# Optimization experiments

Measured on AMD Instinct MI355X. Metric: run time of the kernel, lower is better.

## Reference

```python
import jax, jax.numpy as jnp
import numpy as np

DIM = 1024
HEADS = 16
DIM_HEAD = 64
NUM_FREQS = 16
INNER = HEADS * DIM_HEAD


def rotate_half(x):
    # matches torch: cat((-x[..., 1::2], x[..., ::2]), dim=-1)
    x1 = x[..., ::2]
    x2 = x[..., 1::2]
    return jnp.concatenate((-x2, x1), axis=-1)


def rope_fourier_cache(seq_len, head_dim, num_freqs):
    freqs = 10000.0 ** (-jnp.arange(0, head_dim, 2, dtype=jnp.float32) / head_dim)  # [hd/2]
    pos = jnp.arange(seq_len, dtype=jnp.float32)[:, None]  # [n,1]
    angles = pos * freqs  # [n, hd/2]
    sin = jnp.sin(angles)
    cos = jnp.cos(angles)
    # interleave-duplicate each value per pair: [n, hd]
    sin = jnp.stack([sin, sin], axis=-1).reshape(seq_len, head_dim)
    cos = jnp.stack([cos, cos], axis=-1).reshape(seq_len, head_dim)
    ffreqs = jnp.arange(1, num_freqs + 1, dtype=jnp.float32)  # [F]
    p = jnp.arange(seq_len, dtype=jnp.float32)[:, None]  # [n,1]
    fourier = jnp.concatenate([jnp.sin(p * ffreqs), jnp.cos(p * ffreqs)], axis=-1)  # [n, 2F]
    return sin, cos, fourier


def setup_inputs() -> dict:
    key = jax.random.key(0)
    ks = jax.random.split(key, 6)
    b, n = 4, 2048
    x = jax.random.normal(ks[0], (b, n, DIM), dtype=jnp.float32)
    w_qkv = jax.random.normal(ks[1], (3 * INNER, DIM), dtype=jnp.float32) * (DIM ** -0.5)
    w_fproj = jax.random.normal(ks[2], (DIM_HEAD, 2 * NUM_FREQS), dtype=jnp.float32) * ((2 * NUM_FREQS) ** -0.5)
    b_fproj = jax.random.normal(ks[3], (DIM_HEAD,), dtype=jnp.float32) * 0.02
    w_out = jax.random.normal(ks[4], (DIM, INNER), dtype=jnp.float32) * (INNER ** -0.5)
    b_out = jax.random.normal(ks[5], (DIM,), dtype=jnp.float32) * 0.02
    return {"x": x, "w_qkv": w_qkv, "w_fproj": w_fproj, "b_fproj": b_fproj,
            "w_out": w_out, "b_out": b_out}


def reference(x, w_qkv, w_fproj, b_fproj, w_out, b_out):
    b, n, _ = x.shape
    scale = DIM_HEAD ** -0.5
    qkv = x @ w_qkv.T  # [b, n, 3*inner]
    q, k, v = jnp.split(qkv, 3, axis=-1)
    def to_heads(t):
        return t.reshape(b, n, HEADS, DIM_HEAD).transpose(0, 2, 1, 3)  # [b,h,n,d]
    q, k, v = to_heads(q), to_heads(k), to_heads(v)
    sin, cos, fourier = rope_fourier_cache(n, DIM_HEAD, NUM_FREQS)
    fenc = fourier @ w_fproj.T + b_fproj  # [n, d]
    fenc = fenc[None, None]  # [1,1,n,d]
    q = q * cos + rotate_half(q) * sin + fenc
    k = k * cos + rotate_half(k) * sin + fenc
    dots = jnp.einsum('bhid,bhjd->bhij', q, k) * scale
    attn = jax.nn.softmax(dots, axis=-1)
    out = jnp.einsum('bhij,bhjd->bhid', attn, v)
    out = out.transpose(0, 2, 1, 3).reshape(b, n, INNER)
    return out @ w_out.T + b_out
```

## Files before the change

### kernel.cpp

```cpp
#include <hip/hip_runtime.h>
#include <math.h>

#define NB 4
#define SEQ 2048
#define DIMM 1024
#define NH 16
#define DHD 64
#define NFQ 16

typedef __bf16 bf16x8 __attribute__((ext_vector_type(8)));
typedef __bf16 bf16x4 __attribute__((ext_vector_type(4)));
typedef float f32x4 __attribute__((ext_vector_type(4)));
typedef float f32x16 __attribute__((ext_vector_type(16)));
typedef unsigned int u32x4 __attribute__((ext_vector_type(4)));

#if __has_builtin(__builtin_amdgcn_exp2f)
#define EXP2F(x) __builtin_amdgcn_exp2f(x)
#else
#define EXP2F(x) exp2f(x)
#endif

__device__ inline unsigned short f2bf(float f) {
  unsigned int u = __builtin_bit_cast(unsigned int, f);
  u += 0x7fffu + ((u >> 16) & 1u);
  return (unsigned short)(u >> 16);
}

#define GLL16(gp, lp) __builtin_amdgcn_global_load_lds( \
    (__attribute__((address_space(1))) void*)(gp), \
    (__attribute__((address_space(3))) void*)(lp), 16, 0, 0)

__global__ __launch_bounds__(64) void rope_tab_kernel(const float* __restrict__ w_fproj,
                                                      const float* __restrict__ b_fproj,
                                                      float4* __restrict__ tab) {
  const int pos = blockIdx.x;
  const int d = threadIdx.x;
  __shared__ float four[2 * NFQ];
  if (d < NFQ) {
    double a = (double)pos * (double)(d + 1);
    four[d] = (float)sin(a);
    four[d + NFQ] = (float)cos(a);
  }
  __syncthreads();
  float fe = b_fproj[d];
  const float* wr = w_fproj + d * 2 * NFQ;
#pragma unroll
  for (int j = 0; j < 2 * NFQ; ++j) fe += four[j] * wr[j];
  const int i = d >> 1;
  const double freq = exp(((double)(-2 * i)) / 64.0 * log(10000.0));
  const float angle = (float)pos * (float)freq;
  const float c = (float)cos((double)angle);
  const float s = (float)sin((double)angle);
  tab[(pos << 6) + d] = make_float4(c, s, fe, 0.f);
}

__global__ __launch_bounds__(256) void f2bf_kernel(const float* __restrict__ src,
                                                   unsigned short* __restrict__ dst, int n4) {
  for (int i = blockIdx.x * 256 + threadIdx.x; i < n4; i += gridDim.x * 256) {
    const float4 v = ((const float4*)src)[i];
    ushort4 o;
    o.x = f2bf(v.x); o.y = f2bf(v.y); o.z = f2bf(v.z); o.w = f2bf(v.w);
    ((ushort4*)dst)[i] = o;
  }
}

template<int EPI>
__global__ __launch_bounds__(256) void gemm_bt(const unsigned short* __restrict__ A,
                                               const unsigned short* __restrict__ Bw,
                                               int K,
                                               float* __restrict__ outF,
                                               unsigned short* __restrict__ outQ,
                                               unsigned short* __restrict__ outK,
                                               unsigned short* __restrict__ outV,
                                               const float4* __restrict__ tab,
                                               const float* __restrict__ bias,
                                               float qscale) {
  __shared__ __align__(16) unsigned short As[3][128 * 32];
  __shared__ __align__(16) unsigned short Bs[3][128 * 32];
  const int t = threadIdx.x, l = t & 63, w = t >> 6;
  const int wr = w >> 1, wc = w & 1;
  const int orig = blockIdx.x + gridDim.x * blockIdx.y;
  const int xcd = orig & 7, idx = orig >> 3;
  const int sc = idx >> 5, r5 = idx & 31;
  const int bm = ((xcd << 3) + (r5 >> 2)) * 128;
  const int bn = ((sc << 2) + (r5 & 3)) * 128;
  const f32x4 z = {0.f, 0.f, 0.f, 0.f};
  f32x4 acc[4][4];
#pragma unroll
  for (int m = 0; m < 4; ++m)
#pragma unroll
    for (int n = 0; n < 4; ++n) acc[m][n] = z;

  auto stage = [&](int k0, int buf) {
#pragma unroll
    for (int j = 0; j < 2; ++j) {
      const int Bb = w * 2048 + j * 1024 + l * 16;
      const int row = Bb >> 6, bin = Bb & 63;
      const int sb = bin ^ ((row & 3) << 4);
      GLL16(A  + (size_t)(bm + row) * K + k0 + (sb >> 1), (char*)(&As[buf][0]) + w * 2048 + j * 1024);
      GLL16(Bw + (size_t)(bn + row) * K + k0 + (sb >> 1), (char*)(&Bs[buf][0]) + w * 2048 + j * 1024);
    }
  };

  const int NT = K >> 5;
  stage(0, 0);
  if (NT > 1) stage(32, 1);
  if (NT > 2) stage(64, 2);
  int cur = 0;
  for (int it = 0; it < NT; ++it) {
    const int rem = NT - 1 - it;
    if (rem >= 2)      asm volatile("s_waitcnt vmcnt(8)" ::: "memory");
    else if (rem == 1) asm volatile("s_waitcnt vmcnt(4)" ::: "memory");
    else               asm volatile("s_waitcnt vmcnt(0)" ::: "memory");
    __builtin_amdgcn_s_barrier();

    bf16x8 af[4], bfr[4];
#pragma unroll
    for (int m = 0; m < 4; ++m) {
      const int row = wr * 64 + m * 16 + (l & 15);
      const int bin = ((l >> 4) * 16) ^ ((row & 3) << 4);
      af[m] = *(const bf16x8*)((const char*)(&As[cur][0]) + row * 64 + bin);
    }
#pragma unroll
    for (int n = 0; n < 4; ++n) {
      const int row = wc * 64 + n * 16 + (l & 15);
      const int bin = ((l >> 4) * 16) ^ ((row & 3) << 4);
      bfr[n] = *(const bf16x8*)((const char*)(&Bs[cur][0]) + row * 64 + bin);
    }
#pragma unroll
    for (int m = 0; m < 4; ++m)
#pragma unroll
      for (int n = 0; n < 4; ++n)
        acc[m][n] = __builtin_amdgcn_mfma_f32_16x16x32_bf16(af[m], bfr[n], acc[m][n], 0, 0, 0);

    asm volatile("s_waitcnt lgkmcnt(0)" ::: "memory");
    __builtin_amdgcn_s_barrier();
    if (it + 3 < NT) stage((it + 3) * 32, cur);
    cur = (cur == 2) ? 0 : cur + 1;
  }

  const int c = l & 15;
  if (EPI == 0) {
    const int which = bn >> 10;
    const int h = ((bn & 1023) >> 6) + wc;
    if (which == 2) {
#pragma unroll
      for (int m = 0; m < 4; ++m)
#pragma unroll
        for (int n = 0; n < 4; ++n) {
          const int d = n * 16 + c;
#pragma unroll
          for (int r = 0; r < 4; ++r) {
            const int mrow = bm + wr * 64 + m * 16 + (l >> 4) * 4 + r;
            const int b = mrow >> 11, pos = mrow & (SEQ - 1);
            outV[((size_t)(b * NH + h) * DHD + d) * SEQ + pos] = f2bf(acc[m][n][r]);
          }
        }
    } else {
      unsigned short* dst = (which == 0) ? outQ : outK;
      const float sc2 = (which == 0) ? qscale : 1.f;
      const int laneE = (l & 48) | ((2 * c) & 15);
      const int laneO = (l & 48) | ((2 * c + 1) & 15);
      const bool hi = (c >= 8);
#pragma unroll
      for (int m = 0; m < 4; ++m)
#pragma unroll
        for (int r = 0; r < 4; ++r) {
          const int mrow = bm + wr * 64 + m * 16 + (l >> 4) * 4 + r;
          const int b = mrow >> 11, pos = mrow & (SEQ - 1);
          const float V0 = acc[m][0][r], V1 = acc[m][1][r];
          const float V2 = acc[m][2][r], V3 = acc[m][3][r];
          const float e0 = __shfl(V0, laneE), e1 = __shfl(V1, laneE);
          const float e2 = __shfl(V2, laneE), e3 = __shfl(V3, laneE);
          const float o0 = __shfl(V0, laneO), o1 = __shfl(V1, laneO);
          const float o2 = __shfl(V2, laneO), o3 = __shfl(V3, laneO);
          const float rot0 = -(hi ? o1 : o0);
          const float rot1 = -(hi ? o3 : o2);
          const float rot2 =  (hi ? e1 : e0);
          const float rot3 =  (hi ? e3 : e2);
          const float4 t0 = tab[(pos << 6) + c];
          const float4 t1 = tab[(pos << 6) + 16 + c];
          const float4 t2 = tab[(pos << 6) + 32 + c];
          const float4 t3 = tab[(pos << 6) + 48 + c];
          unsigned short* drow = dst + ((size_t)(b * NH + h) * SEQ + pos) * DHD + c;
          drow[0]  = f2bf((V0 * t0.x + rot0 * t0.y + t0.z) * sc2);
          drow[16] = f2bf((V1 * t1.x + rot1 * t1.y + t1.z) * sc2);
          drow[32] = f2bf((V2 * t2.x + rot2 * t2.y + t2.z) * sc2);
          drow[48] = f2bf((V3 * t3.x + rot3 * t3.y + t3.z) * sc2);
        }
    }
  } else {
#pragma unroll
    for (int m = 0; m < 4; ++m)
#pragma unroll
      for (int n = 0; n < 4; ++n) {
        const int ncol = bn + wc * 64 + n * 16 + c;
        const float bb = bias[ncol];
#pragma unroll
        for (int r = 0; r < 4; ++r) {
          const int mrow = bm + wr * 64 + m * 16 + (l >> 4) * 4 + r;
          outF[(size_t)mrow * DIMM + ncol] = acc[m][n][r] + bb;
        }
      }
  }
}

__global__ __launch_bounds__(256, 2) void attn_kernel(const unsigned short* __restrict__ qbf,
                                                      const unsigned short* __restrict__ kbf,
                                                      const unsigned short* __restrict__ vt,
                                                      unsigned short* __restrict__ ao) {
  __shared__ __align__(16) unsigned short Ks[2][64 * 64], Vts[2][64 * 64];
  __shared__ float ltab[4][64];
  const int t = threadIdx.x, l = t & 63, w = t >> 6;
  const int G = l >> 5, c32 = l & 31;
  int flat = blockIdx.x + (blockIdx.y << 3);
  flat = (flat & 7) * 64 + (flat >> 3);
  const int q0 = (flat & 7) * 256;
  const int bh = flat >> 3;
  const int b = bh >> 4, h = bh & 15;
  const size_t hbase = (size_t)bh * SEQ * DHD;
  const int woff = w * 64;

  auto stageKV = [&](int kt, int buf) {
#pragma unroll
    for (int j = 0; j < 2; ++j) {
      const int base = (w * 2 + j) * 1024;
      const int row = (base + l * 16) >> 7;
      const int sb = ((l & 7) * 16) ^ ((row & 7) << 4);
      GLL16(kbf + hbase + (size_t)(kt + row) * DHD + (sb >> 1),
            (char*)(&Ks[buf][0]) + base);
      GLL16(vt  + hbase + (size_t)row * SEQ + kt + (sb >> 1),
            (char*)(&Vts[buf][0]) + base);
    }
  };

  bf16x8 qf[2][4];
#pragma unroll
  for (int qg = 0; qg < 2; ++qg)
#pragma unroll
    for (int j = 0; j < 4; ++j)
      qf[qg][j] = *(const bf16x8*)(qbf + hbase +
          (size_t)(q0 + woff + qg * 32 + c32) * DHD + 16 * j + 8 * G);

  stageKV(0, 0);
  stageKV(64, 1);

  f32x16 of[2][2];
  float psum[2] = {0.f, 0.f};
#pragma unroll
  for (int qg = 0; qg < 2; ++qg)
#pragma unroll
    for (int dg = 0; dg < 2; ++dg)
#pragma unroll
      for (int r = 0; r < 16; ++r) of[qg][dg][r] = 0.f;

  for (int kt = 0; kt < SEQ; kt += 64) {
    const int cur = (kt >> 6) & 1;
    if (kt + 64 < SEQ) asm volatile("s_waitcnt vmcnt(4)" ::: "memory");
    else               asm volatile("s_waitcnt vmcnt(0)" ::: "memory");
    __builtin_amdgcn_s_barrier();

    const char* Kc = (const char*)(&Ks[cur][0]);
    const char* Vc = (const char*)(&Vts[cur][0]);

#pragma unroll
    for (int ksub = 0; ksub < 2; ++ksub) {
      f32x16 sf0, sf1;
#pragma unroll
      for (int r = 0; r < 16; ++r) { sf0[r] = 0.f; sf1[r] = 0.f; }
      const int krow = ksub * 32 + c32;
      const int kswz = (krow & 7) << 4;
      __builtin_amdgcn_s_setprio(1);
#pragma unroll
      for (int j = 0; j < 4; ++j) {
        const bf16x8 kf = *(const bf16x8*)(Kc + krow * 128 + ((32 * j + 16 * G) ^ kswz));
        sf0 = __builtin_amdgcn_mfma_f32_32x32x16_bf16(kf, qf[0][j], sf0, 0, 0, 0);
        sf1 = __builtin_amdgcn_mfma_f32_32x32x16_bf16(kf, qf[1][j], sf1, 0, 0, 0);
      }
      __builtin_amdgcn_s_setprio(0);

      bf16x8 pa[2][2];
#pragma unroll
      for (int qg = 0; qg < 2; ++qg) {
        const f32x16 sv = qg ? sf1 : sf0;
        float p[16];
#pragma unroll
        for (int r = 0; r < 16; ++r) p[r] = EXP2F(sv[r]);
        float s0 = 0.f;
#pragma unroll
        for (int r = 0; r < 16; ++r) s0 += p[r];
        psum[qg] += s0;
        unsigned W[8];
#pragma unroll
        for (int a = 0; a < 4; ++a)
#pragma unroll
          for (int hh = 0; hh < 2; ++hh)
            asm("v_cvt_pk_bf16_f32 %0, %1, %2"
                : "=v"(W[a * 2 + hh]) : "v"(p[4 * a + 2 * hh]), "v"(p[4 * a + 2 * hh + 1]));
#pragma unroll
        for (int m = 0; m < 2; ++m) {
          const unsigned sendA = G ? W[4 * m + 0] : W[4 * m + 2];
          const unsigned sendB = G ? W[4 * m + 1] : W[4 * m + 3];
          const unsigned rA = (unsigned)__shfl_xor((int)sendA, 32);
          const unsigned rB = (unsigned)__shfl_xor((int)sendB, 32);
          const unsigned w0 = G ? rA : W[4 * m + 0];
          const unsigned w1 = G ? rB : W[4 * m + 1];
          const unsigned w2 = G ? W[4 * m + 2] : rA;
          const unsigned w3 = G ? W[4 * m + 3] : rB;
          const u32x4 tmp = {w0, w1, w2, w3};
          pa[qg][m] = __builtin_bit_cast(bf16x8, tmp);
        }
      }

      const int vrow0 = c32, vrow1 = 32 + c32;
      const int vswz0 = (vrow0 & 7) << 4, vswz1 = (vrow1 & 7) << 4;
      __builtin_amdgcn_s_setprio(1);
#pragma unroll
      for (int m = 0; m < 2; ++m) {
        const int vb = 64 * ksub + 32 * m + 16 * G;
        const bf16x8 vf0 = *(const bf16x8*)(Vc + vrow0 * 128 + (vb ^ vswz0));
        const bf16x8 vf1 = *(const bf16x8*)(Vc + vrow1 * 128 + (vb ^ vswz1));
        of[0][0] = __builtin_amdgcn_mfma_f32_32x32x16_bf16(pa[0][m], vf0, of[0][0], 0, 0, 0);
        of[1][0] = __builtin_amdgcn_mfma_f32_32x32x16_bf16(pa[1][m], vf0, of[1][0], 0, 0, 0);
        of[0][1] = __builtin_amdgcn_mfma_f32_32x32x16_bf16(pa[0][m], vf1, of[0][1], 0, 0, 0);
        of[1][1] = __builtin_amdgcn_mfma_f32_32x32x16_bf16(pa[1][m], vf1, of[1][1], 0, 0, 0);
      }
      __builtin_amdgcn_s_setprio(0);
    }

    asm volatile("s_waitcnt lgkmcnt(0)" ::: "memory");
    __builtin_amdgcn_s_barrier();
    if (kt + 128 < SEQ) stageKV(kt + 128, cur);
  }

#pragma unroll
  for (int qg = 0; qg < 2; ++qg) {
    const float tot = psum[qg] + __shfl_xor(psum[qg], 32);
    if (l < 32) ltab[w][qg * 32 + c32] = tot;
  }

#pragma unroll
  for (int qg = 0; qg < 2; ++qg) {
#pragma unroll
    for (int r = 0; r < 16; ++r) {
      const int qrow = (r & 3) + 8 * (r >> 2) + 4 * G;
      const float inv = 1.f / ltab[w][qg * 32 + qrow];
      const int pos = q0 + woff + qg * 32 + qrow;
#pragma unroll
      for (int dg = 0; dg < 2; ++dg) {
        const int col = h * DHD + dg * 32 + c32;
        ao[((size_t)(b * SEQ + pos)) * DIMM + col] = f2bf(of[qg][dg][r] * inv);
      }
    }
  }
}

extern "C" void kernel_launch(void* const* d_in, const int* in_sizes, int n_in,
                              void* d_out, int out_size, void* d_ws, size_t ws_size,
                              hipStream_t stream) {
  const float* x       = (const float*)d_in[0];
  const float* w_qkv   = (const float*)d_in[1];
  const float* w_fproj = (const float*)d_in[2];
  const float* b_fproj = (const float*)d_in[3];
  const float* w_out   = (const float*)d_in[4];
  const float* b_out   = (const float*)d_in[5];
  char* ws = (char*)d_ws;

  unsigned short* qbf    = (unsigned short*)(ws);
  unsigned short* kbf    = (unsigned short*)(ws + 16777216);
  unsigned short* vt     = (unsigned short*)(ws + 33554432);
  unsigned short* xbf    = (unsigned short*)(ws + 50331648);
  unsigned short* aobf   = (unsigned short*)(ws + 67108864);
  unsigned short* wqkvbf = (unsigned short*)(ws + 83886080);
  unsigned short* woutbf = (unsigned short*)(ws + 90177536);
  float4*         tab    = (float4*)(ws + 92274688);

  const float kLog2e = 1.4426950408889634f;

  hipLaunchKernelGGL(rope_tab_kernel, dim3(SEQ), dim3(DHD), 0, stream, w_fproj, b_fproj, tab);
  hipLaunchKernelGGL(f2bf_kernel, dim3(2048), dim3(256), 0, stream, x, xbf, (NB*SEQ*DIMM)/4);
  hipLaunchKernelGGL(f2bf_kernel, dim3(768), dim3(256), 0, stream, w_qkv, wqkvbf, (3*DIMM*DIMM)/4);
  hipLaunchKernelGGL(f2bf_kernel, dim3(256), dim3(256), 0, stream, w_out, woutbf, (DIMM*DIMM)/4);
  hipLaunchKernelGGL((gemm_bt<0>), dim3(24, 64), dim3(256), 0, stream,
                     xbf, wqkvbf, DIMM, (float*)nullptr, qbf, kbf, vt, tab,
                     (const float*)nullptr, 0.125f * kLog2e);
  hipLaunchKernelGGL(attn_kernel, dim3(SEQ/256, NB*NH), dim3(256), 0, stream, qbf, kbf, vt, aobf);
  hipLaunchKernelGGL((gemm_bt<1>), dim3(8, 64), dim3(256), 0, stream,
                     aobf, woutbf, DIMM, (float*)d_out, (unsigned short*)nullptr,
                     (unsigned short*)nullptr, (unsigned short*)nullptr, (const float4*)nullptr,
                     b_out, 1.0f);
}
```

Measured before the change: 196.8 us.

## Halve attention query tile per wave and compute row sums via MFMA

Each attention block now covers 128 query rows (32 per wave) instead of 256, doubling the grid and raising the launch-bounds occupancy hint from 2 to 4 blocks. The softmax denominator is now accumulated with an extra MFMA against a ones vector, replacing the scalar sums, shuffles and LDS table. The goal is lower register pressure and more waves in flight to hide latency. The cost is twice the K/V staging traffic per query and one extra MFMA for every two PV MFMAs.

Result: slower. 201.9 us (+2.6%).

```diff
diff --git a/kernel.cpp b/kernel.cpp
--- a/kernel.cpp
+++ b/kernel.cpp
@@ -9,7 +9,6 @@
 #define NFQ 16
 
 typedef __bf16 bf16x8 __attribute__((ext_vector_type(8)));
-typedef __bf16 bf16x4 __attribute__((ext_vector_type(4)));
 typedef float f32x4 __attribute__((ext_vector_type(4)));
 typedef float f32x16 __attribute__((ext_vector_type(16)));
 typedef unsigned int u32x4 __attribute__((ext_vector_type(4)));
@@ -205,21 +204,24 @@
   }
 }
 
-__global__ __launch_bounds__(256, 2) void attn_kernel(const unsigned short* __restrict__ qbf,
+__global__ __launch_bounds__(256, 4) void attn_kernel(const unsigned short* __restrict__ qbf,
                                                       const unsigned short* __restrict__ kbf,
                                                       const unsigned short* __restrict__ vt,
                                                       unsigned short* __restrict__ ao) {
   __shared__ __align__(16) unsigned short Ks[2][64 * 64], Vts[2][64 * 64];
-  __shared__ float ltab[4][64];
   const int t = threadIdx.x, l = t & 63, w = t >> 6;
   const int G = l >> 5, c32 = l & 31;
-  int flat = blockIdx.x + (blockIdx.y << 3);
-  flat = (flat & 7) * 64 + (flat >> 3);
-  const int q0 = (flat & 7) * 256;
-  const int bh = flat >> 3;
+  int flat = blockIdx.x + (blockIdx.y << 4);
+  flat = (flat & 7) * 128 + (flat >> 3);
+  const int q0 = (flat & 15) * 128;
+  const int bh = flat >> 4;
   const int b = bh >> 4, h = bh & 15;
   const size_t hbase = (size_t)bh * SEQ * DHD;
-  const int woff = w * 64;
+  const int woff = w * 32;
+
+  bf16x8 ones;
+#pragma unroll
+  for (int j = 0; j < 8; ++j) ones[j] = (__bf16)1.0f;
 
   auto stageKV = [&](int kt, int buf) {
 #pragma unroll
@@ -234,25 +236,18 @@
     }
   };
 
-  bf16x8 qf[2][4];
-#pragma unroll
-  for (int qg = 0; qg < 2; ++qg)
-#pragma unroll
-    for (int j = 0; j < 4; ++j)
-      qf[qg][j] = *(const bf16x8*)(qbf + hbase +
-          (size_t)(q0 + woff + qg * 32 + c32) * DHD + 16 * j + 8 * G);
+  bf16x8 qf[4];
+#pragma unroll
+  for (int j = 0; j < 4; ++j)
+    qf[j] = *(const bf16x8*)(qbf + hbase +
+        (size_t)(q0 + woff + c32) * DHD + 16 * j + 8 * G);
 
   stageKV(0, 0);
   stageKV(64, 1);
 
-  f32x16 of[2][2];
-  float psum[2] = {0.f, 0.f};
-#pragma unroll
-  for (int qg = 0; qg < 2; ++qg)
-#pragma unroll
-    for (int dg = 0; dg < 2; ++dg)
-#pragma unroll
-      for (int r = 0; r < 16; ++r) of[qg][dg][r] = 0.f;
+  f32x16 of[2], lsum;
+#pragma unroll
+  for (int r = 0; r < 16; ++r) { of[0][r] = 0.f; of[1][r] = 0.f; lsum[r] = 0.f; }
 
   for (int kt = 0; kt < SEQ; kt += 64) {
     const int cur = (kt >> 6) & 1;
@@ -265,51 +260,42 @@
 
 #pragma unroll
     for (int ksub = 0; ksub < 2; ++ksub) {
-      f32x16 sf0, sf1;
-#pragma unroll
-      for (int r = 0; r < 16; ++r) { sf0[r] = 0.f; sf1[r] = 0.f; }
+      f32x16 sf;
+#pragma unroll
+      for (int r = 0; r < 16; ++r) sf[r] = 0.f;
       const int krow = ksub * 32 + c32;
       const int kswz = (krow & 7) << 4;
       __builtin_amdgcn_s_setprio(1);
 #pragma unroll
       for (int j = 0; j < 4; ++j) {
         const bf16x8 kf = *(const bf16x8*)(Kc + krow * 128 + ((32 * j + 16 * G) ^ kswz));
-        sf0 = __builtin_amdgcn_mfma_f32_32x32x16_bf16(kf, qf[0][j], sf0, 0, 0, 0);
-        sf1 = __builtin_amdgcn_mfma_f32_32x32x16_bf16(kf, qf[1][j], sf1, 0, 0, 0);
+        sf = __builtin_amdgcn_mfma_f32_32x32x16_bf16(kf, qf[j], sf, 0, 0, 0);
       }
       __builtin_amdgcn_s_setprio(0);
 
-      bf16x8 pa[2][2];
-#pragma unroll
-      for (int qg = 0; qg < 2; ++qg) {
-        const f32x16 sv = qg ? sf1 : sf0;
-        float p[16];
-#pragma unroll
-        for (int r = 0; r < 16; ++r) p[r] = EXP2F(sv[r]);
-        float s0 = 0.f;
-#pragma unroll
-        for (int r = 0; r < 16; ++r) s0 += p[r];
-        psum[qg] += s0;
-        unsigned W[8];
-#pragma unroll
-        for (int a = 0; a < 4; ++a)
-#pragma unroll
-          for (int hh = 0; hh < 2; ++hh)
-            asm("v_cvt_pk_bf16_f32 %0, %1, %2"
-                : "=v"(W[a * 2 + hh]) : "v"(p[4 * a + 2 * hh]), "v"(p[4 * a + 2 * hh + 1]));
-#pragma unroll
-        for (int m = 0; m < 2; ++m) {
-          const unsigned sendA = G ? W[4 * m + 0] : W[4 * m + 2];
-          const unsigned sendB = G ? W[4 * m + 1] : W[4 * m + 3];
-          const unsigned rA = (unsigned)__shfl_xor((int)sendA, 32);
-          const unsigned rB = (unsigned)__shfl_xor((int)sendB, 32);
-          const unsigned w0 = G ? rA : W[4 * m + 0];
-          const unsigned w1 = G ? rB : W[4 * m + 1];
-          const unsigned w2 = G ? W[4 * m + 2] : rA;
-          const unsigned w3 = G ? W[4 * m + 3] : rB;
-          const u32x4 tmp = {w0, w1, w2, w3};
-          pa[qg][m] = __builtin_bit_cast(bf16x8, tmp);
-        }
+      float p[16];
+#pragma unroll
+      for (int r = 0; r < 16; ++r) p[r] = EXP2F(sf[r]);
+      unsigned W[8];
+#pragma unroll
+      for (int a = 0; a < 4; ++a)
+#pragma unroll
+        for (int hh = 0; hh < 2; ++hh)
+          asm("v_cvt_pk_bf16_f32 %0, %1, %2"
+              : "=v"(W[a * 2 + hh]) : "v"(p[4 * a + 2 * hh]), "v"(p[4 * a + 2 * hh + 1]));
+      bf16x8 pa[2];
+#pragma unroll
+      for (int m = 0; m < 2; ++m) {
+        const unsigned sendA = G ? W[4 * m + 0] : W[4 * m + 2];
+        const unsigned sendB = G ? W[4 * m + 1] : W[4 * m + 3];
+        const unsigned rA = (unsigned)__shfl_xor((int)sendA, 32);
+        const unsigned rB = (unsigned)__shfl_xor((int)sendB, 32);
+        const unsigned w0 = G ? rA : W[4 * m + 0];
+        const unsigned w1 = G ? rB : W[4 * m + 1];
+        const unsigned w2 = G ? W[4 * m + 2] : rA;
+        const unsigned w3 = G ? W[4 * m + 3] : rB;
+        const u32x4 tmp = {w0, w1, w2, w3};
+        pa[m] = __builtin_bit_cast(bf16x8, tmp);
       }
 
       const int vrow0 = c32, vrow1 = 32 + c32;
@@ -317,13 +303,12 @@
       __builtin_amdgcn_s_setprio(1);
 #pragma unroll
       for (int m = 0; m < 2; ++m) {
+        lsum = __builtin_amdgcn_mfma_f32_32x32x16_bf16(pa[m], ones, lsum, 0, 0, 0);
         const int vb = 64 * ksub + 32 * m + 16 * G;
         const bf16x8 vf0 = *(const bf16x8*)(Vc + vrow0 * 128 + (vb ^ vswz0));
         const bf16x8 vf1 = *(const bf16x8*)(Vc + vrow1 * 128 + (vb ^ vswz1));
-        of[0][0] = __builtin_amdgcn_mfma_f32_32x32x16_bf16(pa[0][m], vf0, of[0][0], 0, 0, 0);
-        of[1][0] = __builtin_amdgcn_mfma_f32_32x32x16_bf16(pa[1][m], vf0, of[1][0], 0, 0, 0);
-        of[0][1] = __builtin_amdgcn_mfma_f32_32x32x16_bf16(pa[0][m], vf1, of[0][1], 0, 0, 0);
-        of[1][1] = __builtin_amdgcn_mfma_f32_32x32x16_bf16(pa[1][m], vf1, of[1][1], 0, 0, 0);
+        of[0] = __builtin_amdgcn_mfma_f32_32x32x16_bf16(pa[m], vf0, of[0], 0, 0, 0);
+        of[1] = __builtin_amdgcn_mfma_f32_32x32x16_bf16(pa[m], vf1, of[1], 0, 0, 0);
       }
       __builtin_amdgcn_s_setprio(0);
     }
@@ -334,23 +319,14 @@
   }
 
 #pragma unroll
-  for (int qg = 0; qg < 2; ++qg) {
-    const float tot = psum[qg] + __shfl_xor(psum[qg], 32);
-    if (l < 32) ltab[w][qg * 32 + c32] = tot;
-  }
-
-#pragma unroll
-  for (int qg = 0; qg < 2; ++qg) {
-#pragma unroll
-    for (int r = 0; r < 16; ++r) {
-      const int qrow = (r & 3) + 8 * (r >> 2) + 4 * G;
-      const float inv = 1.f / ltab[w][qg * 32 + qrow];
-      const int pos = q0 + woff + qg * 32 + qrow;
-#pragma unroll
-      for (int dg = 0; dg < 2; ++dg) {
-        const int col = h * DHD + dg * 32 + c32;
-        ao[((size_t)(b * SEQ + pos)) * DIMM + col] = f2bf(of[qg][dg][r] * inv);
-      }
+  for (int r = 0; r < 16; ++r) {
+    const int qrow = (r & 3) + 8 * (r >> 2) + 4 * G;
+    const float inv = 1.f / lsum[r];
+    const int pos = q0 + woff + qrow;
+#pragma unroll
+    for (int dg = 0; dg < 2; ++dg) {
+      const int col = h * DHD + dg * 32 + c32;
+      ao[((size_t)(b * SEQ + pos)) * DIMM + col] = f2bf(of[dg][r] * inv);
     }
   }
 }
@@ -384,7 +360,7 @@
   hipLaunchKernelGGL((gemm_bt<0>), dim3(24, 64), dim3(256), 0, stream,
                      xbf, wqkvbf, DIMM, (float*)nullptr, qbf, kbf, vt, tab,
                      (const float*)nullptr, 0.125f * kLog2e);
-  hipLaunchKernelGGL(attn_kernel, dim3(SEQ/256, NB*NH), dim3(256), 0, stream, qbf, kbf, vt, aobf);
+  hipLaunchKernelGGL(attn_kernel, dim3(SEQ/128, NB*NH), dim3(256), 0, stream, qbf, kbf, vt, aobf);
   hipLaunchKernelGGL((gemm_bt<1>), dim3(8, 64), dim3(256), 0, stream,
                      aobf, woutbf, DIMM, (float*)d_out, (unsigned short*)nullptr,
                      (unsigned short*)nullptr, (unsigned short*)nullptr, (const float4*)nullptr,
```
